# Kernel optimization log

Hardware: AMD Instinct MI355X
Metric: run time of the kernel (lower is better)

The kernel has to match this reference:

```python
import jax, jax.numpy as jnp
import numpy as np

B, D, M, R, C = 4096, 16, 4, 2048, 10
EPS = 1e-9


def setup_inputs() -> dict:
    key = jax.random.key(0)
    k1, k2, k3, k4, k5 = jax.random.split(key, 5)
    x = jax.random.normal(k1, (B, D), dtype=jnp.float32)
    centers = jax.random.normal(k2, (D, M), dtype=jnp.float32)
    widths = jax.random.uniform(k3, (D, M), dtype=jnp.float32, minval=0.5, maxval=1.5)
    consequents = jax.random.uniform(k4, (R, D + 1, C), dtype=jnp.float32)
    rules = jax.random.randint(k5, (R, D), 0, M, dtype=jnp.int32)
    return {"x": x, "centers": centers, "widths": widths,
            "consequents": consequents, "rules": rules}


def reference(x, centers, widths, consequents, rules):
    batch = x.shape[0]
    # Gaussian membership values: (B, D, M)
    mfs = jnp.exp(-((x[:, :, None] - centers[None]) ** 2) / (2.0 * widths[None] ** 2))
    # Gather per-rule memberships: rule_mfs[b, d, r] = mfs[b, d, rules[r, d]] -> (B, D, R)
    idx = jnp.broadcast_to(rules.T[None].astype(jnp.int32), (batch, rules.shape[1], rules.shape[0]))
    rule_mfs = jnp.take_along_axis(mfs, idx, axis=2)
    # Firing strengths: product over input dims -> (B, R)
    fs = jnp.prod(rule_mfs, axis=1)
    norm_fs = fs / (jnp.sum(fs, axis=1, keepdims=True) + EPS)
    # Extended input with bias column -> (B, D+1)
    x_ext = jnp.concatenate([x, jnp.ones((batch, 1), dtype=x.dtype)], axis=1)
    # Faithful to torch.einsum('bi,rjc->brc', ...): i and j are both summed out
    rule_vals = jnp.einsum('bi,rjc->brc', x_ext, consequents)  # (B, R, C)
    out = jnp.einsum('br,brc->bc', norm_fs, rule_vals)  # (B, C)
    return out, norm_fs, x_ext
```

## Files before the change

kernel.cpp:

```cpp
#include <hip/hip_runtime.h>

#define BB 4096
#define DD 16
#define MM 4
#define RR 2048
#define CC 10
#define TB 4
#define RPT (RR / 256)

typedef __attribute__((ext_vector_type(4))) float f32x4;

__global__ __launch_bounds__(256) void prep_kernel(
    const float* __restrict__ cons, const int* __restrict__ rules,
    float* __restrict__ wsumT, unsigned int* __restrict__ codes)
{
    int gid = blockIdx.x * 256 + threadIdx.x;
    if (gid < RR * CC) {
        int r = gid / CC, c = gid - r * CC;
        const float* cr = cons + (size_t)r * (DD + 1) * CC + c;
        float s = 0.0f;
#pragma unroll
        for (int j = 0; j < DD + 1; ++j) s += cr[j * CC];
        wsumT[c * RR + r] = s;
    }
    if (gid < RR) {
        const int* rrp = rules + gid * DD;
        unsigned int code = 0;
#pragma unroll
        for (int g = 0; g < 4; ++g) {
            unsigned int byt = 0;
#pragma unroll
            for (int k = 0; k < 4; ++k)
                byt |= (((unsigned int)rrp[g * 4 + k]) & 3u) << (2 * k);
            code |= byt << (8 * g);
        }
        codes[gid] = code;
    }
}

__global__ __launch_bounds__(256) void anfis_main(
    const float* __restrict__ x, const float* __restrict__ centers,
    const float* __restrict__ widths, const float* __restrict__ wsumT,
    const unsigned int* __restrict__ codes,
    float* __restrict__ out, float* __restrict__ norm_fs, float* __restrict__ x_ext)
{
    __shared__ float MF[TB][64];
    __shared__ f32x4 PAIR4[8][16];
    __shared__ f32x4 QUAD4[4][256];
    __shared__ float RED[TB * CC][68];
    __shared__ float xs[TB][DD];
    __shared__ float sx[TB];
    __shared__ float wpart[4][TB];
    __shared__ float invl[TB];
    __shared__ float oscale[TB];
    __shared__ float part2[TB * CC][4];

    const int tid = threadIdx.x;
    const int b0 = blockIdx.x * TB;
    const int lane = tid & 63;
    const int wv = tid >> 6;

    if (tid < TB * DD) {
        int row = tid / DD, d = tid % DD;
        float v = x[(b0 + row) * DD + d];
        xs[row][d] = v;
        x_ext[(b0 + row) * (DD + 1) + d] = v;
    }
    if (tid < TB) x_ext[(b0 + tid) * (DD + 1) + DD] = 1.0f;
    __syncthreads();

    if (tid < TB) {
        float s = 1.0f;
#pragma unroll
        for (int d = 0; d < DD; ++d) s += xs[tid][d];
        sx[tid] = s;
    }

    {
        int row = tid >> 6, dm = tid & 63, d = dm >> 2, m = dm & 3;
        float c = centers[d * MM + m];
        float w = widths[d * MM + m];
        float z = xs[row][d] - c;
        MF[row][dm] = expf(-(z * z) / (2.0f * w * w));
    }
    __syncthreads();

    if (tid < 8 * 16) {
        int p = tid >> 4, e = tid & 15;
        int i0 = e & 3, i1 = e >> 2;
        f32x4 v;
#pragma unroll
        for (int row = 0; row < TB; ++row)
            v[row] = MF[row][(2 * p) * 4 + i0] * MF[row][(2 * p + 1) * 4 + i1];
        PAIR4[p][e] = v;
    }
    __syncthreads();

#pragma unroll
    for (int i = tid; i < 4 * 256; i += 256) {
        int g = i >> 8, e = i & 255;
        QUAD4[g][e] = PAIR4[2 * g][e & 15] * PAIR4[2 * g + 1][e >> 4];
    }
    __syncthreads();

    float fsreg[TB][RPT];
    float acc[TB][CC];
    float ssum[TB];
#pragma unroll
    for (int row = 0; row < TB; ++row) {
        ssum[row] = 0.0f;
#pragma unroll
        for (int c = 0; c < CC; ++c) acc[row][c] = 0.0f;
    }

#pragma unroll
    for (int j = 0; j < RPT; ++j) {
        int r = tid + 256 * j;
        unsigned int code = codes[r];
        float w[CC];
#pragma unroll
        for (int c = 0; c < CC; ++c) w[c] = wsumT[c * RR + r];
        f32x4 q0 = QUAD4[0][code & 255u];
        f32x4 q1 = QUAD4[1][(code >> 8) & 255u];
        f32x4 q2 = QUAD4[2][(code >> 16) & 255u];
        f32x4 q3 = QUAD4[3][code >> 24];
#pragma unroll
        for (int row = 0; row < TB; ++row) {
            float fs = (q0[row] * q1[row]) * (q2[row] * q3[row]);
            fsreg[row][j] = fs;
            ssum[row] += fs;
#pragma unroll
            for (int c = 0; c < CC; ++c) acc[row][c] = fmaf(fs, w[c], acc[row][c]);
        }
    }

#pragma unroll
    for (int row = 0; row < TB; ++row) {
        float s = ssum[row];
#pragma unroll
        for (int off = 32; off > 0; off >>= 1) s += __shfl_xor(s, off, 64);
        if (lane == 0) wpart[wv][row] = s;
    }
    __syncthreads();
    if (tid < TB) {
        float t = wpart[0][tid] + wpart[1][tid] + wpart[2][tid] + wpart[3][tid];
        float inv = 1.0f / (t + 1e-9f);
        invl[tid] = inv;
        oscale[tid] = sx[tid] * inv;
    }
    __syncthreads();

#pragma unroll
    for (int row = 0; row < TB; ++row) {
        float inv = invl[row];
#pragma unroll
        for (int j = 0; j < RPT; ++j) {
            norm_fs[(size_t)(b0 + row) * RR + tid + 256 * j] = fsreg[row][j] * inv;
        }
    }

#pragma unroll
    for (int row = 0; row < TB; ++row) {
#pragma unroll
        for (int c = 0; c < CC; ++c) {
            float s = acc[row][c];
            s += __shfl_xor(s, 1, 64);
            s += __shfl_xor(s, 2, 64);
            if ((lane & 3) == 0) RED[row * CC + c][wv * 16 + (lane >> 2)] = s;
        }
    }
    __syncthreads();
    if (tid < 160) {
        int v = tid % 40, ch = tid / 40;
        float s = 0.0f;
        int base = ch * 16;
#pragma unroll
        for (int i = 0; i < 16; ++i) s += RED[v][base + i];
        part2[v][ch] = s;
    }
    __syncthreads();
    if (tid < TB * CC) {
        float val = part2[tid][0] + part2[tid][1] + part2[tid][2] + part2[tid][3];
        int row = tid / CC, c = tid % CC;
        out[(b0 + row) * CC + c] = oscale[row] * val;
    }
}

extern "C" void kernel_launch(void* const* d_in, const int* in_sizes, int n_in,
                              void* d_out, int out_size, void* d_ws, size_t ws_size,
                              hipStream_t stream) {
    const float* x       = (const float*)d_in[0];
    const float* centers = (const float*)d_in[1];
    const float* widths  = (const float*)d_in[2];
    const float* cons    = (const float*)d_in[3];
    const int*   rules   = (const int*)d_in[4];

    float* out_p     = (float*)d_out;
    float* norm_fs_p = out_p + (size_t)BB * CC;
    float* x_ext_p   = norm_fs_p + (size_t)BB * RR;

    float* wsumT = (float*)d_ws;
    unsigned int* codes = (unsigned int*)((char*)d_ws + (size_t)CC * RR * sizeof(float));

    prep_kernel<<<(RR * CC + 255) / 256, 256, 0, stream>>>(cons, rules, wsumT, codes);
    anfis_main<<<BB / TB, 256, 0, stream>>>(x, centers, widths, wsumT, codes,
                                            out_p, norm_fs_p, x_ext_p);
}
```

Baseline: 91.00 us.

## Halve batch tile and recompute firing strengths to cut register pressure

Drops the batch tile from four rows to two per block and stops holding all firing strengths in registers. Strengths are computed once to get the normaliser, then recomputed in a second pass that writes normalized values and accumulates outputs. The consequent sums are repacked row-major as float4/float4/float2 so each rule's weights load with vector instructions, and shared memory is aliased between the quad table and the reduction buffer. The aim is higher occupancy (launch bounds request 8 blocks) at the cost of duplicated table lookups and twice as many blocks, each re-reading the codes and weights.

```diff
diff --git a/kernel.cpp b/kernel.cpp
--- a/kernel.cpp
+++ b/kernel.cpp
@@ -5,14 +5,16 @@
 #define MM 4
 #define RR 2048
 #define CC 10
-#define TB 4
+#define TB 2
 #define RPT (RR / 256)
 
 typedef __attribute__((ext_vector_type(4))) float f32x4;
+typedef __attribute__((ext_vector_type(2))) float f32x2;
 
 __global__ __launch_bounds__(256) void prep_kernel(
     const float* __restrict__ cons, const int* __restrict__ rules,
-    float* __restrict__ wsumT, unsigned int* __restrict__ codes)
+    float* __restrict__ wsum4a, float* __restrict__ wsum4b,
+    float* __restrict__ wsum2, unsigned int* __restrict__ codes)
 {
     int gid = blockIdx.x * 256 + threadIdx.x;
     if (gid < RR * CC) {
@@ -21,7 +23,9 @@
         float s = 0.0f;
 #pragma unroll
         for (int j = 0; j < DD + 1; ++j) s += cr[j * CC];
-        wsumT[c * RR + r] = s;
+        if (c < 4)      wsum4a[r * 4 + c] = s;
+        else if (c < 8) wsum4b[r * 4 + (c - 4)] = s;
+        else            wsum2[r * 2 + (c - 8)] = s;
     }
     if (gid < RR) {
         const int* rrp = rules + gid * DD;
@@ -38,16 +42,19 @@
     }
 }
 
-__global__ __launch_bounds__(256) void anfis_main(
+__global__ __launch_bounds__(256, 8) void anfis_main(
     const float* __restrict__ x, const float* __restrict__ centers,
-    const float* __restrict__ widths, const float* __restrict__ wsumT,
+    const float* __restrict__ widths, const f32x4* __restrict__ wsum4a,
+    const f32x4* __restrict__ wsum4b, const f32x2* __restrict__ wsum2,
     const unsigned int* __restrict__ codes,
     float* __restrict__ out, float* __restrict__ norm_fs, float* __restrict__ x_ext)
 {
+    __shared__ __align__(16) char pool[4 * 256 * sizeof(f32x2)];
+    f32x2 (*Q2)[256] = (f32x2 (*)[256])pool;
+    float (*RED)[68] = (float (*)[68])pool;
+
     __shared__ float MF[TB][64];
-    __shared__ f32x4 PAIR4[8][16];
-    __shared__ f32x4 QUAD4[4][256];
-    __shared__ float RED[TB * CC][68];
+    __shared__ f32x2 PAIR2[8][16];
     __shared__ float xs[TB][DD];
     __shared__ float sx[TB];
     __shared__ float wpart[4][TB];
@@ -60,15 +67,13 @@
     const int lane = tid & 63;
     const int wv = tid >> 6;
 
-    if (tid < TB * DD) {
-        int row = tid / DD, d = tid % DD;
-        float v = x[(b0 + row) * DD + d];
-        xs[row][d] = v;
-        x_ext[(b0 + row) * (DD + 1) + d] = v;
-    }
-    if (tid < TB) x_ext[(b0 + tid) * (DD + 1) + DD] = 1.0f;
-    __syncthreads();
-
+    if (tid < TB * (DD + 1)) {
+        int row = tid / (DD + 1), col = tid % (DD + 1);
+        float v = (col < DD) ? x[(b0 + row) * DD + col] : 1.0f;
+        if (col < DD) xs[row][col] = v;
+        x_ext[(b0 + row) * (DD + 1) + col] = v;
+    }
+    __syncthreads();
     if (tid < TB) {
         float s = 1.0f;
 #pragma unroll
@@ -76,7 +81,7 @@
         sx[tid] = s;
     }
 
-    {
+    if (tid < TB * 64) {
         int row = tid >> 6, dm = tid & 63, d = dm >> 2, m = dm & 3;
         float c = centers[d * MM + m];
         float w = widths[d * MM + m];
@@ -88,58 +93,41 @@
     if (tid < 8 * 16) {
         int p = tid >> 4, e = tid & 15;
         int i0 = e & 3, i1 = e >> 2;
-        f32x4 v;
-#pragma unroll
-        for (int row = 0; row < TB; ++row)
-            v[row] = MF[row][(2 * p) * 4 + i0] * MF[row][(2 * p + 1) * 4 + i1];
-        PAIR4[p][e] = v;
+        f32x2 v;
+        v.x = MF[0][(2 * p) * 4 + i0] * MF[0][(2 * p + 1) * 4 + i1];
+        v.y = MF[1][(2 * p) * 4 + i0] * MF[1][(2 * p + 1) * 4 + i1];
+        PAIR2[p][e] = v;
     }
     __syncthreads();
 
 #pragma unroll
     for (int i = tid; i < 4 * 256; i += 256) {
         int g = i >> 8, e = i & 255;
-        QUAD4[g][e] = PAIR4[2 * g][e & 15] * PAIR4[2 * g + 1][e >> 4];
-    }
-    __syncthreads();
-
-    float fsreg[TB][RPT];
-    float acc[TB][CC];
-    float ssum[TB];
-#pragma unroll
-    for (int row = 0; row < TB; ++row) {
-        ssum[row] = 0.0f;
-#pragma unroll
-        for (int c = 0; c < CC; ++c) acc[row][c] = 0.0f;
-    }
-
-#pragma unroll
+        Q2[g][e] = PAIR2[2 * g][e & 15] * PAIR2[2 * g + 1][e >> 4];
+    }
+    __syncthreads();
+
+    float ssum0 = 0.0f, ssum1 = 0.0f;
+#pragma unroll 1
     for (int j = 0; j < RPT; ++j) {
-        int r = tid + 256 * j;
-        unsigned int code = codes[r];
-        float w[CC];
-#pragma unroll
-        for (int c = 0; c < CC; ++c) w[c] = wsumT[c * RR + r];
-        f32x4 q0 = QUAD4[0][code & 255u];
-        f32x4 q1 = QUAD4[1][(code >> 8) & 255u];
-        f32x4 q2 = QUAD4[2][(code >> 16) & 255u];
-        f32x4 q3 = QUAD4[3][code >> 24];
-#pragma unroll
-        for (int row = 0; row < TB; ++row) {
-            float fs = (q0[row] * q1[row]) * (q2[row] * q3[row]);
-            fsreg[row][j] = fs;
-            ssum[row] += fs;
-#pragma unroll
-            for (int c = 0; c < CC; ++c) acc[row][c] = fmaf(fs, w[c], acc[row][c]);
-        }
-    }
-
-#pragma unroll
-    for (int row = 0; row < TB; ++row) {
-        float s = ssum[row];
-#pragma unroll
-        for (int off = 32; off > 0; off >>= 1) s += __shfl_xor(s, off, 64);
-        if (lane == 0) wpart[wv][row] = s;
+        unsigned int code = codes[tid + 256 * j];
+        f32x2 q0 = Q2[0][code & 255u];
+        f32x2 q1 = Q2[1][(code >> 8) & 255u];
+        f32x2 q2 = Q2[2][(code >> 16) & 255u];
+        f32x2 q3 = Q2[3][code >> 24];
+        f32x2 p = (q0 * q1) * (q2 * q3);
+        ssum0 += p.x;
+        ssum1 += p.y;
+    }
+
+    {
+        float s0 = ssum0, s1 = ssum1;
+#pragma unroll
+        for (int off = 32; off > 0; off >>= 1) {
+            s0 += __shfl_xor(s0, off, 64);
+            s1 += __shfl_xor(s1, off, 64);
+        }
+        if (lane == 0) { wpart[wv][0] = s0; wpart[wv][1] = s1; }
     }
     __syncthreads();
     if (tid < TB) {
@@ -150,14 +138,39 @@
     }
     __syncthreads();
 
-#pragma unroll
-    for (int row = 0; row < TB; ++row) {
-        float inv = invl[row];
-#pragma unroll
-        for (int j = 0; j < RPT; ++j) {
-            norm_fs[(size_t)(b0 + row) * RR + tid + 256 * j] = fsreg[row][j] * inv;
-        }
-    }
+    const float inv0 = invl[0], inv1 = invl[1];
+
+    float acc[TB][CC];
+#pragma unroll
+    for (int row = 0; row < TB; ++row)
+#pragma unroll
+        for (int c = 0; c < CC; ++c) acc[row][c] = 0.0f;
+
+#pragma unroll 1
+    for (int j = 0; j < RPT; ++j) {
+        int r = tid + 256 * j;
+        unsigned int code = codes[r];
+        f32x2 q0 = Q2[0][code & 255u];
+        f32x2 q1 = Q2[1][(code >> 8) & 255u];
+        f32x2 q2 = Q2[2][(code >> 16) & 255u];
+        f32x2 q3 = Q2[3][code >> 24];
+        f32x2 p = (q0 * q1) * (q2 * q3);
+
+        norm_fs[(size_t)(b0 + 0) * RR + r] = p.x * inv0;
+        norm_fs[(size_t)(b0 + 1) * RR + r] = p.y * inv1;
+
+        const f32x4 wa = wsum4a[r];
+        const f32x4 wb = wsum4b[r];
+        const f32x2 wcp = wsum2[r];
+        const float wc[CC] = {wa.x, wa.y, wa.z, wa.w, wb.x,
+                              wb.y, wb.z, wb.w, wcp.x, wcp.y};
+#pragma unroll
+        for (int c = 0; c < CC; ++c) {
+            acc[0][c] = fmaf(p.x, wc[c], acc[0][c]);
+            acc[1][c] = fmaf(p.y, wc[c], acc[1][c]);
+        }
+    }
+    __syncthreads();
 
 #pragma unroll
     for (int row = 0; row < TB; ++row) {
@@ -170,8 +183,8 @@
         }
     }
     __syncthreads();
-    if (tid < 160) {
-        int v = tid % 40, ch = tid / 40;
+    if (tid < 80) {
+        int v = tid % 20, ch = tid / 20;
         float s = 0.0f;
         int base = ch * 16;
 #pragma unroll
@@ -199,10 +212,16 @@
     float* norm_fs_p = out_p + (size_t)BB * CC;
     float* x_ext_p   = norm_fs_p + (size_t)BB * RR;
 
-    float* wsumT = (float*)d_ws;
-    unsigned int* codes = (unsigned int*)((char*)d_ws + (size_t)CC * RR * sizeof(float));
-
-    prep_kernel<<<(RR * CC + 255) / 256, 256, 0, stream>>>(cons, rules, wsumT, codes);
-    anfis_main<<<BB / TB, 256, 0, stream>>>(x, centers, widths, wsumT, codes,
+    float* wsum4a = (float*)d_ws;
+    float* wsum4b = wsum4a + (size_t)RR * 4;
+    float* wsum2  = wsum4b + (size_t)RR * 4;
+    unsigned int* codes = (unsigned int*)(wsum2 + (size_t)RR * 2);
+
+    prep_kernel<<<(RR * CC + 255) / 256, 256, 0, stream>>>(cons, rules, wsum4a,
+                                                           wsum4b, wsum2, codes);
+    anfis_main<<<BB / TB, 256, 0, stream>>>(x, centers, widths,
+                                            (const f32x4*)wsum4a,
+                                            (const f32x4*)wsum4b,
+                                            (const f32x2*)wsum2, codes,
                                             out_p, norm_fs_p, x_ext_p);
 }
```

New measurement: 89.55 us. About the same (-1.6%).
